# Optimization experiments

Hardware: AMD Instinct MI355X
Metric: run time of the kernel (lower is better)

The kernel has to match this reference:

```python
import jax, jax.numpy as jnp
import numpy as np

N = 50000
E = 800000
D_IN = 128
D_HID = 256


def setup_inputs() -> dict:
    key = jax.random.key(0)
    ks = jax.random.split(key, 9)
    x = jax.random.normal(ks[0], (N, D_IN), dtype=jnp.float32)
    edge_index = jax.random.randint(ks[1], (2, E), 0, N, dtype=jnp.int64)
    edge_weight = jax.random.uniform(ks[2], (E,), dtype=jnp.float32)
    # GCNConv params (lin: y = x @ W.T, plus bias added after aggregation)
    W1 = jax.random.normal(ks[3], (D_HID, D_IN), dtype=jnp.float32) / np.sqrt(D_IN)
    b1 = jnp.zeros((D_HID,), dtype=jnp.float32)
    W2 = jax.random.normal(ks[4], (D_IN, D_HID), dtype=jnp.float32) / np.sqrt(D_HID)
    b2 = jnp.zeros((D_IN,), dtype=jnp.float32)
    gamma = jnp.ones((D_IN,), dtype=jnp.float32)
    beta = jnp.zeros((D_IN,), dtype=jnp.float32)
    return {"x": x, "edge_index": edge_index, "edge_weight": edge_weight,
            "W1": W1, "b1": b1, "W2": W2, "b2": b2,
            "gamma": gamma, "beta": beta}


def _gcn_norm(edge_index, edge_weight, n_nodes):
    # add self loops with weight 1.0 (PyG gcn_norm default)
    loop = jnp.arange(n_nodes, dtype=edge_index.dtype)
    src = jnp.concatenate([edge_index[0], loop])
    dst = jnp.concatenate([edge_index[1], loop])
    w = jnp.concatenate([edge_weight, jnp.ones((n_nodes,), edge_weight.dtype)])
    # symmetric normalization: deg over target index
    deg = jax.ops.segment_sum(w, dst, num_segments=n_nodes)
    dinv = jnp.where(deg > 0, jax.lax.rsqrt(deg), 0.0)
    norm = dinv[src] * w * dinv[dst]
    return src, dst, norm


def _gcn_conv(x, src, dst, norm, W, b, n_nodes):
    h = x @ W.T                                    # [N, out]
    msg = h[src] * norm[:, None]                   # gather + scale [E+N, out]
    out = jax.ops.segment_sum(msg, dst, num_segments=n_nodes)
    return out + b


def reference(x, edge_index, edge_weight, W1, b1, W2, b2, gamma, beta):
    n_nodes = x.shape[0]
    src, dst, norm = _gcn_norm(edge_index, edge_weight, n_nodes)
    h = _gcn_conv(x, src, dst, norm, W1, b1, n_nodes)
    h = jax.nn.relu(h)
    h = _gcn_conv(h, src, dst, norm, W2, b2, n_nodes)
    # LayerNorm over last dim
    mu = jnp.mean(h, axis=-1, keepdims=True)
    var = jnp.mean(jnp.square(h - mu), axis=-1, keepdims=True)
    h = (h - mu) * jax.lax.rsqrt(var + 1e-5) * gamma + beta
    return h
```

## Files before the change

### kernel.cpp

```cpp
#include <hip/hip_runtime.h>

typedef unsigned short ushort_t;
typedef unsigned long long u64_t;
typedef __attribute__((ext_vector_type(8))) short short8;
typedef __attribute__((ext_vector_type(4))) float float4v;

__device__ inline float b2f(ushort_t u) {
    unsigned x = ((unsigned)u) << 16;
    return __builtin_bit_cast(float, x);
}
__device__ inline ushort_t f2b(float f) {
    unsigned x = __builtin_bit_cast(unsigned, f);
    unsigned r = (x + 0x7fffu + ((x >> 16) & 1u)) >> 16;
    return (ushort_t)r;
}

__device__ inline void load_edge(const int* __restrict__ ei, int e, int E,
                                 int& s, int& d) {
    int ec = min(e, E - 1);
    int2 c64 = ((const int2*)ei)[ec];
    unsigned long long m = __ballot(c64.y != 0);
    if (m != 0ull) {
        s = ei[ec];
        d = ei[(size_t)E + ec];
    } else {
        s = c64.x;
        d = ((const int2*)ei)[(size_t)E + ec].x;
    }
}


__global__ __launch_bounds__(256) void k_mega(const int* __restrict__ ei,
                                              const float* __restrict__ w,
                                              const float* __restrict__ x,
                                              const float* __restrict__ W1,
                                              const float* __restrict__ W2,
                                              u64_t* packed, int* __restrict__ rank,
                                              ushort_t* __restrict__ xb,
                                              ushort_t* __restrict__ W1b,
                                              ushort_t* __restrict__ W2b,
                                              int E, int Nn, int gE, int gX) {
    int b = blockIdx.x;
    if (b < gE) {
        int e = b * 256 + threadIdx.x;
        int s, d;
        load_edge(ei, e, E, s, d);
        if (e < E) {
            if ((unsigned)s < (unsigned)Nn && (unsigned)d < (unsigned)Nn) {
                unsigned fx = (unsigned)(w[e] * 16777216.0f + 0.5f);
                u64_t old = atomicAdd(packed + d, (1ull << 32) | (u64_t)fx);
                rank[e] = (int)(old >> 32);
            } else {
                rank[e] = -1;
            }
        }
    } else if (b < gE + gX) {
        int i = (b - gE) * 256 + threadIdx.x;
        if (i < Nn * 32) {
            float4v v = ((const float4v*)x)[i];
            ushort4 o;
            o.x = f2b(v[0]); o.y = f2b(v[1]); o.z = f2b(v[2]); o.w = f2b(v[3]);
            ((ushort4*)xb)[i] = o;
        }
    } else {
        int i = (b - gE - gX) * 256 + threadIdx.x;
        if (i < 32768) W1b[i] = f2b(W1[i]);
        else if (i < 65536) W2b[i - 32768] = f2b(W2[i - 32768]);
    }
}

__device__ inline int cnt_hi(const u64_t* packed, int i) {
    return ((const int*)packed)[2 * i + 1];
}


__global__ __launch_bounds__(256) void k_scan_a(const u64_t* __restrict__ packed,
                                                int* __restrict__ bsum, int Nn) {
    int b = blockIdx.x, t = threadIdx.x;
    int base = b * 2048 + t * 8;
    int s = 0;
#pragma unroll
    for (int j = 0; j < 8; ++j) { int i = base + j; if (i < Nn) s += cnt_hi(packed, i); }
#pragma unroll
    for (int off = 1; off < 64; off <<= 1) s += __shfl_xor(s, off);
    __shared__ int wsum[4];
    if ((t & 63) == 0) wsum[t >> 6] = s;
    __syncthreads();
    if (t == 0) bsum[b] = wsum[0] + wsum[1] + wsum[2] + wsum[3];
}

__global__ void k_scan_b(const int* __restrict__ bsum, int* __restrict__ bbase,
                         int nb, int* __restrict__ offs, int Nn) {
    int t = threadIdx.x;
    int own = (t < nb) ? bsum[t] : 0;
    int v = own;
#pragma unroll
    for (int off = 1; off < 64; off <<= 1) {
        int u = __shfl_up(v, off);
        if (t >= off) v += u;
    }
    if (t < nb) bbase[t] = v - own;
    if (t == 63) offs[Nn] = v;
}

__global__ __launch_bounds__(256) void k_scan_c(const u64_t* __restrict__ packed,
                                                const int* __restrict__ bbase,
                                                int* __restrict__ offs,
                                                float* __restrict__ dinv, int Nn) {
    int b = blockIdx.x, t = threadIdx.x;
    int base = b * 2048 + t * 8;
    u64_t pk[8];
    int v[8];
    int s = 0;
#pragma unroll
    for (int j = 0; j < 8; ++j) {
        int i = base + j;
        pk[j] = (i < Nn) ? packed[i] : 0ull;
        v[j] = (int)(pk[j] >> 32);
        s += v[j];
    }
    __shared__ int sd[256];
    sd[t] = s;
    __syncthreads();
    for (int off = 1; off < 256; off <<= 1) {
        int u = (t >= off) ? sd[t - off] : 0;
        __syncthreads();
        sd[t] += u;
        __syncthreads();
    }
    int pos = bbase[b] + sd[t] - s;
#pragma unroll
    for (int j = 0; j < 8; ++j) {
        int i = base + j;
        if (i < Nn) {
            offs[i] = pos; pos += v[j];
            float deg = 1.0f + (float)(unsigned)(pk[j] & 0xFFFFFFFFull) * (1.0f / 16777216.0f);
            dinv[i] = rsqrtf(deg);
        }
    }
}


__global__ void k_scatter(const int* __restrict__ ei, const float* __restrict__ w,
                          const float* __restrict__ dinv,
                          const int* __restrict__ offs,
                          const int* __restrict__ rank,
                          int2* __restrict__ edata, int E, int Nn) {
    int e = blockIdx.x * 256 + threadIdx.x;
    int s, d;
    load_edge(ei, e, E, s, d);
    if (e >= E) return;
    int r = rank[e];
    if (r < 0) return;
    int pos = offs[d] + r;
    float nw = dinv[s] * w[e] * dinv[d];
    int2 p;
    p.x = s;
    p.y = __builtin_bit_cast(int, nw);
    edata[pos] = p;
}


__device__ inline void agg_edges(const ushort_t* __restrict__ src,
                                 const int2* __restrict__ edata,
                                 int s, int e, int hl, int p, float* a) {
    int i = s;
    for (; i + 7 < e; i += 8) {
#pragma unroll
        for (int j = 0; j < 4; ++j) {
            int idx = i + p + 2 * j;
            int2 ed = edata[idx];
            float nw = __builtin_bit_cast(float, ed.y);
            ushort4 q = ((const ushort4*)(src + (size_t)ed.x * 128))[hl];
            a[0] += b2f(q.x) * nw; a[1] += b2f(q.y) * nw;
            a[2] += b2f(q.z) * nw; a[3] += b2f(q.w) * nw;
        }
    }
    for (; i < e; i += 2) {
        int idx = i + p;
        int ic = min(idx, e - 1);
        int2 ed = edata[ic];
        float nw = (idx < e) ? __builtin_bit_cast(float, ed.y) : 0.f;
        ushort4 q = ((const ushort4*)(src + (size_t)ed.x * 128))[hl];
        a[0] += b2f(q.x) * nw; a[1] += b2f(q.y) * nw;
        a[2] += b2f(q.z) * nw; a[3] += b2f(q.w) * nw;
    }
}

__global__ __launch_bounds__(256) void k_agg1(const ushort_t* __restrict__ xb,
                                              const int* __restrict__ offs,
                                              const int2* __restrict__ edata,
                                              const float* __restrict__ dinv,
                                              ushort_t* __restrict__ ax, int Nn) {
    int v = (blockIdx.x * blockDim.x + threadIdx.x) >> 6;
    int lane = threadIdx.x & 63;
    if (v >= Nn) return;
    int hl = lane & 31, p = lane >> 5;
    float a[4] = {0.f, 0.f, 0.f, 0.f};
    if (p == 0) {
        float dv = dinv[v];
        float sn = dv * dv;
        ushort4 pq = ((const ushort4*)(xb + (size_t)v * 128))[hl];
        a[0] = b2f(pq.x) * sn; a[1] = b2f(pq.y) * sn;
        a[2] = b2f(pq.z) * sn; a[3] = b2f(pq.w) * sn;
    }
    int s = offs[v], e = offs[v + 1];
    agg_edges(xb, edata, s, e, hl, p, a);
#pragma unroll
    for (int j = 0; j < 4; ++j) a[j] += __shfl_xor(a[j], 32);
    if (p == 0) {
        ushort4 o;
        o.x = f2b(a[0]); o.y = f2b(a[1]); o.z = f2b(a[2]); o.w = f2b(a[3]);
        ((ushort4*)(ax + (size_t)v * 128))[hl] = o;
    }
}


__global__ __launch_bounds__(256, 2) void k_gemm_fused(const ushort_t* __restrict__ ax,
                                                       const ushort_t* __restrict__ W1b,
                                                       const float* __restrict__ b1v,
                                                       const ushort_t* __restrict__ W2b,
                                                       ushort_t* __restrict__ h2, int Nn) {
    __shared__ ushort_t tile[64][264];
    int tid = threadIdx.x, wid = tid >> 6, lane = tid & 63;
    int m = lane & 15, q = lane >> 4;
    int blk = blockIdx.x * 64;

    short8 wf[4][4];
#pragma unroll
    for (int nt = 0; nt < 4; ++nt) {
        const ushort_t* wb = W1b + (size_t)(wid * 64 + nt * 16 + m) * 128 + q * 8;
#pragma unroll
        for (int kt = 0; kt < 4; ++kt) wf[nt][kt] = *(const short8*)(wb + kt * 32);
    }
    short8 af[4][4];
#pragma unroll
    for (int mi = 0; mi < 4; ++mi) {
        int arow = blk + mi * 16 + m;
        bool rv = arow < Nn;
        const ushort_t* ab = ax + (size_t)arow * 128 + q * 8;
#pragma unroll
        for (int kt = 0; kt < 4; ++kt)
            af[mi][kt] = rv ? *(const short8*)(ab + kt * 32) : (short8)0;
    }

    float4v acc1[4][4];
#pragma unroll
    for (int mi = 0; mi < 4; ++mi)
#pragma unroll
        for (int nt = 0; nt < 4; ++nt) acc1[mi][nt] = (float4v){0.f, 0.f, 0.f, 0.f};

#pragma unroll
    for (int kt = 0; kt < 4; ++kt)
#pragma unroll
        for (int mi = 0; mi < 4; ++mi)
#pragma unroll
            for (int nt = 0; nt < 4; ++nt)
                acc1[mi][nt] = __builtin_amdgcn_mfma_f32_16x16x32_bf16(
                    af[mi][kt], wf[nt][kt], acc1[mi][nt], 0, 0, 0);

#pragma unroll
    for (int nt = 0; nt < 4; ++nt) {
        int col = wid * 64 + nt * 16 + m;
        float bb = b1v[col];
#pragma unroll
        for (int mi = 0; mi < 4; ++mi) {
#pragma unroll
            for (int r = 0; r < 4; ++r) {
                float v = acc1[mi][nt][r] + bb;
                v = v > 0.f ? v : 0.f;
                tile[mi * 16 + q * 4 + r][col] = f2b(v);
            }
        }
    }
    __syncthreads();

    short8 w2f[2][8];
#pragma unroll
    for (int n2 = 0; n2 < 2; ++n2) {
        const ushort_t* wb = W2b + (size_t)(wid * 32 + n2 * 16 + m) * 256 + q * 8;
#pragma unroll
        for (int kt = 0; kt < 8; ++kt) w2f[n2][kt] = *(const short8*)(wb + kt * 32);
    }

    float4v acc2[4][2];
#pragma unroll
    for (int mi = 0; mi < 4; ++mi)
#pragma unroll
        for (int n2 = 0; n2 < 2; ++n2) acc2[mi][n2] = (float4v){0.f, 0.f, 0.f, 0.f};

#pragma unroll
    for (int kt = 0; kt < 8; ++kt) {
#pragma unroll
        for (int mi = 0; mi < 4; ++mi) {
            short8 a2 = *(const short8*)&tile[mi * 16 + m][kt * 32 + q * 8];
#pragma unroll
            for (int n2 = 0; n2 < 2; ++n2)
                acc2[mi][n2] = __builtin_amdgcn_mfma_f32_16x16x32_bf16(
                    a2, w2f[n2][kt], acc2[mi][n2], 0, 0, 0);
        }
    }

#pragma unroll
    for (int mi = 0; mi < 4; ++mi) {
#pragma unroll
        for (int n2 = 0; n2 < 2; ++n2) {
            int col = wid * 32 + n2 * 16 + m;
#pragma unroll
            for (int r = 0; r < 4; ++r) {
                int row = blk + mi * 16 + q * 4 + r;
                if (row < Nn) h2[(size_t)row * 128 + col] = f2b(acc2[mi][n2][r]);
            }
        }
    }
}


__global__ __launch_bounds__(256) void k_agg2_ln(const ushort_t* __restrict__ h2,
                                                 const int* __restrict__ offs,
                                                 const int2* __restrict__ edata,
                                                 const float* __restrict__ dinv,
                                                 const float* __restrict__ b2v,
                                                 const float* __restrict__ gv,
                                                 const float* __restrict__ bev,
                                                 float* __restrict__ out, int Nn) {
    int v = (blockIdx.x * blockDim.x + threadIdx.x) >> 6;
    int lane = threadIdx.x & 63;
    if (v >= Nn) return;
    int hl = lane & 31, p = lane >> 5;
    float a[4] = {0.f, 0.f, 0.f, 0.f};
    if (p == 0) {
        float dv = dinv[v];
        float sn = dv * dv;
        ushort4 pq = ((const ushort4*)(h2 + (size_t)v * 128))[hl];
        a[0] = b2f(pq.x) * sn; a[1] = b2f(pq.y) * sn;
        a[2] = b2f(pq.z) * sn; a[3] = b2f(pq.w) * sn;
    }
    int s = offs[v], e = offs[v + 1];
    agg_edges(h2, edata, s, e, hl, p, a);
#pragma unroll
    for (int j = 0; j < 4; ++j) a[j] += __shfl_xor(a[j], 32);

    int d0 = hl * 4;
#pragma unroll
    for (int j = 0; j < 4; ++j) a[j] += b2v[d0 + j];

    float ssum = a[0] + a[1] + a[2] + a[3];
    float ssq = a[0] * a[0] + a[1] * a[1] + a[2] * a[2] + a[3] * a[3];
#pragma unroll
    for (int off = 1; off < 64; off <<= 1) {
        ssum += __shfl_xor(ssum, off);
        ssq += __shfl_xor(ssq, off);
    }
    float mu = ssum * (1.0f / 256.0f);
    float var = ssq * (1.0f / 256.0f) - mu * mu;
    float r = rsqrtf(var + 1e-5f);
    if (p == 0) {
        float4v o;
#pragma unroll
        for (int j = 0; j < 4; ++j)
            o[j] = (a[j] - mu) * r * gv[d0 + j] + bev[d0 + j];
        ((float4v*)(out + (size_t)v * 128))[hl] = o;
    }
}


extern "C" void kernel_launch(void* const* d_in, const int* in_sizes, int n_in,
                              void* d_out, int out_size, void* d_ws, size_t ws_size,
                              hipStream_t stream) {
    const float* x   = (const float*)d_in[0];
    const int*   ei  = (const int*)d_in[1];
    const float* ew  = (const float*)d_in[2];
    const float* W1  = (const float*)d_in[3];
    const float* b1v = (const float*)d_in[4];
    const float* W2  = (const float*)d_in[5];
    const float* b2v = (const float*)d_in[6];
    const float* gv  = (const float*)d_in[7];
    const float* bev = (const float*)d_in[8];
    float* out = (float*)d_out;

    const int Nn = in_sizes[0] / 128;
    const int E  = in_sizes[2];

    char* base = (char*)d_ws;
    size_t off = 0;
    auto alloc = [&](size_t bytes) {
        char* p = base + off;
        off = (off + bytes + 255) & ~(size_t)255;
        return p;
    };
    u64_t*  packed = (u64_t*)alloc((size_t)Nn * 8);
    float*  dinv   = (float*)alloc((size_t)Nn * 4);
    int*    offs   = (int*)alloc((size_t)(Nn + 1) * 4);
    int*    bsum   = (int*)alloc(64 * 4);
    int*    bbase  = (int*)alloc(64 * 4);
    int*    rank   = (int*)alloc((size_t)E * 4);
    int2*   edata  = (int2*)alloc((size_t)E * 8);
    ushort_t* xb   = (ushort_t*)alloc((size_t)Nn * 128 * 2);
    ushort_t* h2   = (ushort_t*)alloc((size_t)Nn * 128 * 2);
    ushort_t* W1b  = (ushort_t*)alloc(32768 * 2);
    ushort_t* W2b  = (ushort_t*)alloc(32768 * 2);
    ushort_t* ax   = (ushort_t*)d_out;
    (void)ws_size; (void)n_in; (void)out_size;

    int gE = (E + 255) / 256;
    int gX = (Nn * 32 + 255) / 256;
    int gW = (Nn + 3) / 4;
    int gG = (Nn + 63) / 64;
    int nb = (Nn + 2047) / 2048;

    hipMemsetAsync(packed, 0, (size_t)Nn * 8, stream);
    k_mega<<<gE + gX + 256, 256, 0, stream>>>(ei, ew, x, W1, W2, packed, rank,
                                              xb, W1b, W2b, E, Nn, gE, gX);
    k_scan_a<<<nb, 256, 0, stream>>>(packed, bsum, Nn);
    k_scan_b<<<1, 64, 0, stream>>>(bsum, bbase, nb, offs, Nn);
    k_scan_c<<<nb, 256, 0, stream>>>(packed, bbase, offs, dinv, Nn);
    k_scatter<<<gE, 256, 0, stream>>>(ei, ew, dinv, offs, rank, edata, E, Nn);
    k_agg1<<<gW, 256, 0, stream>>>(xb, offs, edata, dinv, ax, Nn);
    k_gemm_fused<<<gG, 256, 0, stream>>>(ax, W1b, b1v, W2b, h2, Nn);
    k_agg2_ln<<<gW, 256, 0, stream>>>(h2, offs, edata, dinv, b2v, gv, bev, out, Nn);
}
```

Measured before the change: 261.6 us.

## Split aggregation by feature quarter mapped to XCDs for L2 locality

Both aggregation kernels now gather only a 32-feature slice of each neighbour row. Block indices are arranged so that blockIdx mod 8 picks the quarter, which suits the round-robin spread of blocks across the 8 XCDs: each XCD's L2 then only has to hold a quarter of the feature table. Within a wave, four edges are processed in parallel by 16-lane groups and combined with shuffles. LayerNorm moves out of the second aggregation into its own kernel, which reads an intermediate bf16 buffer. The trade-off is four times as many edge-list reads, smaller per-lane gathers, and an extra launch plus an extra pass over memory.

```diff
diff --git a/kernel.cpp b/kernel.cpp
--- a/kernel.cpp
+++ b/kernel.cpp
@@ -161,58 +161,72 @@
 }
 
 
-__device__ inline void agg_edges(const ushort_t* __restrict__ src,
-                                 const int2* __restrict__ edata,
-                                 int s, int e, int hl, int p, float* a) {
+template <bool SELF_SN>
+__device__ inline void agg_quarter(const ushort_t* __restrict__ src,
+                                   const int* __restrict__ offs,
+                                   const int2* __restrict__ edata,
+                                   const float* __restrict__ dinv,
+                                   ushort_t* __restrict__ dst,
+                                   int v, int q, int lane, int Nn) {
+    int grp = lane >> 4, li = lane & 15;
+    int doff = q * 32 + li * 2;
+    float a0 = 0.f, a1 = 0.f;
+    if (grp == 0) {
+        float dv = dinv[v];
+        float sn = dv * dv;
+        ushort2 pq = *(const ushort2*)(src + (size_t)v * 128 + doff);
+        a0 = b2f(pq.x) * sn; a1 = b2f(pq.y) * sn;
+    }
+    int s = offs[v], e = offs[v + 1];
     int i = s;
     for (; i + 7 < e; i += 8) {
-#pragma unroll
-        for (int j = 0; j < 4; ++j) {
-            int idx = i + p + 2 * j;
-            int2 ed = edata[idx];
-            float nw = __builtin_bit_cast(float, ed.y);
-            ushort4 q = ((const ushort4*)(src + (size_t)ed.x * 128))[hl];
-            a[0] += b2f(q.x) * nw; a[1] += b2f(q.y) * nw;
-            a[2] += b2f(q.z) * nw; a[3] += b2f(q.w) * nw;
-        }
-    }
-    for (; i < e; i += 2) {
-        int idx = i + p;
+        int2 e0 = edata[i + grp];
+        int2 e1 = edata[i + 4 + grp];
+        float n0 = __builtin_bit_cast(float, e0.y);
+        float n1 = __builtin_bit_cast(float, e1.y);
+        ushort2 q0 = *(const ushort2*)(src + (size_t)e0.x * 128 + doff);
+        ushort2 q1 = *(const ushort2*)(src + (size_t)e1.x * 128 + doff);
+        a0 += b2f(q0.x) * n0; a1 += b2f(q0.y) * n0;
+        a0 += b2f(q1.x) * n1; a1 += b2f(q1.y) * n1;
+    }
+    for (; i < e; i += 4) {
+        int idx = i + grp;
         int ic = min(idx, e - 1);
         int2 ed = edata[ic];
         float nw = (idx < e) ? __builtin_bit_cast(float, ed.y) : 0.f;
-        ushort4 q = ((const ushort4*)(src + (size_t)ed.x * 128))[hl];
-        a[0] += b2f(q.x) * nw; a[1] += b2f(q.y) * nw;
-        a[2] += b2f(q.z) * nw; a[3] += b2f(q.w) * nw;
-    }
-}
-
-__global__ __launch_bounds__(256) void k_agg1(const ushort_t* __restrict__ xb,
-                                              const int* __restrict__ offs,
-                                              const int2* __restrict__ edata,
-                                              const float* __restrict__ dinv,
-                                              ushort_t* __restrict__ ax, int Nn) {
-    int v = (blockIdx.x * blockDim.x + threadIdx.x) >> 6;
-    int lane = threadIdx.x & 63;
+        ushort2 qq = *(const ushort2*)(src + (size_t)ed.x * 128 + doff);
+        a0 += b2f(qq.x) * nw; a1 += b2f(qq.y) * nw;
+    }
+    a0 += __shfl_xor(a0, 16); a1 += __shfl_xor(a1, 16);
+    a0 += __shfl_xor(a0, 32); a1 += __shfl_xor(a1, 32);
+    if (lane < 16) {
+        ushort2 o; o.x = f2b(a0); o.y = f2b(a1);
+        *(ushort2*)(dst + (size_t)v * 128 + doff) = o;
+    }
+}
+
+__global__ __launch_bounds__(256) void k_agg1q(const ushort_t* __restrict__ xb,
+                                               const int* __restrict__ offs,
+                                               const int2* __restrict__ edata,
+                                               const float* __restrict__ dinv,
+                                               ushort_t* __restrict__ ax, int Nn) {
+    int r = blockIdx.x & 7, g = blockIdx.x >> 3;
+    int q = r >> 1;
+    int v = (g * 2 + (r & 1)) * 4 + (threadIdx.x >> 6);
     if (v >= Nn) return;
-    int hl = lane & 31, p = lane >> 5;
-    float a[4] = {0.f, 0.f, 0.f, 0.f};
-    if (p == 0) {
-        float dv = dinv[v];
-        float sn = dv * dv;
-        ushort4 pq = ((const ushort4*)(xb + (size_t)v * 128))[hl];
-        a[0] = b2f(pq.x) * sn; a[1] = b2f(pq.y) * sn;
-        a[2] = b2f(pq.z) * sn; a[3] = b2f(pq.w) * sn;
-    }
-    int s = offs[v], e = offs[v + 1];
-    agg_edges(xb, edata, s, e, hl, p, a);
-#pragma unroll
-    for (int j = 0; j < 4; ++j) a[j] += __shfl_xor(a[j], 32);
-    if (p == 0) {
-        ushort4 o;
-        o.x = f2b(a[0]); o.y = f2b(a[1]); o.z = f2b(a[2]); o.w = f2b(a[3]);
-        ((ushort4*)(ax + (size_t)v * 128))[hl] = o;
-    }
+    agg_quarter<true>(xb, offs, edata, dinv, ax, v, q, threadIdx.x & 63, Nn);
+}
+
+__global__ __launch_bounds__(256) void k_agg2q(const ushort_t* __restrict__ h2,
+                                               const int* __restrict__ offs,
+                                               const int2* __restrict__ edata,
+                                               const float* __restrict__ dinv,
+                                               ushort_t* __restrict__ a2, int Nn) {
+    int r = blockIdx.x & 7, g = blockIdx.x >> 3;
+    int q = r >> 1;
+    int v = (g * 2 + (r & 1)) * 4 + (threadIdx.x >> 6);
+    if (v >= Nn) return;
+    agg_quarter<true>(h2, offs, edata, dinv, a2, v, q, threadIdx.x & 63, Nn);
 }
 
 
@@ -316,52 +330,31 @@
 }
 
 
-__global__ __launch_bounds__(256) void k_agg2_ln(const ushort_t* __restrict__ h2,
-                                                 const int* __restrict__ offs,
-                                                 const int2* __restrict__ edata,
-                                                 const float* __restrict__ dinv,
-                                                 const float* __restrict__ b2v,
-                                                 const float* __restrict__ gv,
-                                                 const float* __restrict__ bev,
-                                                 float* __restrict__ out, int Nn) {
+__global__ __launch_bounds__(256) void k_ln(const ushort_t* __restrict__ a2,
+                                            const float* __restrict__ b2v,
+                                            const float* __restrict__ gv,
+                                            const float* __restrict__ bev,
+                                            float* __restrict__ out, int Nn) {
     int v = (blockIdx.x * blockDim.x + threadIdx.x) >> 6;
     int lane = threadIdx.x & 63;
     if (v >= Nn) return;
-    int hl = lane & 31, p = lane >> 5;
-    float a[4] = {0.f, 0.f, 0.f, 0.f};
-    if (p == 0) {
-        float dv = dinv[v];
-        float sn = dv * dv;
-        ushort4 pq = ((const ushort4*)(h2 + (size_t)v * 128))[hl];
-        a[0] = b2f(pq.x) * sn; a[1] = b2f(pq.y) * sn;
-        a[2] = b2f(pq.z) * sn; a[3] = b2f(pq.w) * sn;
-    }
-    int s = offs[v], e = offs[v + 1];
-    agg_edges(h2, edata, s, e, hl, p, a);
-#pragma unroll
-    for (int j = 0; j < 4; ++j) a[j] += __shfl_xor(a[j], 32);
-
-    int d0 = hl * 4;
-#pragma unroll
-    for (int j = 0; j < 4; ++j) a[j] += b2v[d0 + j];
-
-    float ssum = a[0] + a[1] + a[2] + a[3];
-    float ssq = a[0] * a[0] + a[1] * a[1] + a[2] * a[2] + a[3] * a[3];
+    int d0 = lane * 2;
+    ushort2 p = ((const ushort2*)(a2 + (size_t)v * 128))[lane];
+    float a0 = b2f(p.x) + b2v[d0];
+    float a1 = b2f(p.y) + b2v[d0 + 1];
+    float ssum = a0 + a1, ssq = a0 * a0 + a1 * a1;
 #pragma unroll
     for (int off = 1; off < 64; off <<= 1) {
         ssum += __shfl_xor(ssum, off);
         ssq += __shfl_xor(ssq, off);
     }
-    float mu = ssum * (1.0f / 256.0f);
-    float var = ssq * (1.0f / 256.0f) - mu * mu;
+    float mu = ssum * (1.0f / 128.0f);
+    float var = ssq * (1.0f / 128.0f) - mu * mu;
     float r = rsqrtf(var + 1e-5f);
-    if (p == 0) {
-        float4v o;
-#pragma unroll
-        for (int j = 0; j < 4; ++j)
-            o[j] = (a[j] - mu) * r * gv[d0 + j] + bev[d0 + j];
-        ((float4v*)(out + (size_t)v * 128))[hl] = o;
-    }
+    float2 o;
+    o.x = (a0 - mu) * r * gv[d0] + bev[d0];
+    o.y = (a1 - mu) * r * gv[d0 + 1] + bev[d0 + 1];
+    ((float2*)(out + (size_t)v * 128))[lane] = o;
 }
 
 
@@ -401,12 +394,14 @@
     ushort_t* W1b  = (ushort_t*)alloc(32768 * 2);
     ushort_t* W2b  = (ushort_t*)alloc(32768 * 2);
     ushort_t* ax   = (ushort_t*)d_out;
+    ushort_t* a2   = xb;
     (void)ws_size; (void)n_in; (void)out_size;
 
     int gE = (E + 255) / 256;
     int gX = (Nn * 32 + 255) / 256;
     int gW = (Nn + 3) / 4;
     int gG = (Nn + 63) / 64;
+    int gQ = 8 * ((Nn + 7) / 8);
     int nb = (Nn + 2047) / 2048;
 
     hipMemsetAsync(packed, 0, (size_t)Nn * 8, stream);
@@ -416,7 +411,8 @@
     k_scan_b<<<1, 64, 0, stream>>>(bsum, bbase, nb, offs, Nn);
     k_scan_c<<<nb, 256, 0, stream>>>(packed, bbase, offs, dinv, Nn);
     k_scatter<<<gE, 256, 0, stream>>>(ei, ew, dinv, offs, rank, edata, E, Nn);
-    k_agg1<<<gW, 256, 0, stream>>>(xb, offs, edata, dinv, ax, Nn);
+    k_agg1q<<<gQ, 256, 0, stream>>>(xb, offs, edata, dinv, ax, Nn);
     k_gemm_fused<<<gG, 256, 0, stream>>>(ax, W1b, b1v, W2b, h2, Nn);
-    k_agg2_ln<<<gW, 256, 0, stream>>>(h2, offs, edata, dinv, b2v, gv, bev, out, Nn);
-}
+    k_agg2q<<<gQ, 256, 0, stream>>>(h2, offs, edata, dinv, a2, Nn);
+    k_ln<<<gW, 256, 0, stream>>>(a2, b2v, gv, bev, out, Nn);
+}
```

Measured after the change: 364.1 us. +39.2%, slower.
